# Kernel optimization log

Hardware: AMD Instinct MI355X
Metric: run time of the kernel (lower is better)

The kernel has to match this reference:

```python
import jax, jax.numpy as jnp
import numpy as np

# Geometry constants from System.__init__ defaults
L0, L1 = 0.4, 0.08                 # drone body half-extent basis lengths (l[0], l[1])
Y_LO, Y_HI = 0.0, 2.0              # y_limits
FAR = 10.0                         # sentinel 'no block ahead' distance
BLOCKS = np.array([[1.0, 0.9, 0.05, 0.4],
                   [2.5, 1.7, 0.05, 0.4],
                   [4.0, 0.4, 0.05, 0.4]], dtype=np.float32)  # [x, y, w, h]
B = 4_194_304                      # batch of environment states


def setup_inputs() -> dict:
    key = jax.random.key(0)
    u = jax.random.uniform(key, (B, 7), dtype=jnp.float32)
    # columns: c_x, c_y, v_x, v_y, phi, theta, wind -> scale to realistic ranges
    scale = jnp.array([5.0, 2.0, 4.0, 4.0, 1.0, 1.0, 2.4], dtype=jnp.float32)
    shift = jnp.array([0.0, 0.0, -2.0, -2.0, -0.5, -0.5, 5.5], dtype=jnp.float32)
    state = u * scale + shift
    blocks = jnp.asarray(BLOCKS)
    return {"state": state, "blocks": blocks}


def _get_observation(state, blocks):
    # state: [B, 7]; faithful vectorization of System.get_observation
    c_x, c_y, v_x, v_y, phi = (state[:, 0], state[:, 1], state[:, 2],
                               state[:, 3], state[:, 4])
    abs_phi = jnp.abs(phi)
    half_x = jnp.cos(phi) * L0 / 2 + jnp.sin(abs_phi) * L1 / 2   # horizontal half-extent
    half_y = jnp.sin(abs_phi) * L0 / 2 + jnp.cos(phi) * L1 / 2   # vertical half-extent

    up = Y_HI - c_y - half_y
    down = c_y - Y_LO - half_y
    d1 = jnp.full_like(c_x, FAR)
    d2 = jnp.full_like(c_x, FAR)

    # small fixed number of blocks -> unrolled loop; later blocks overwrite up/down
    # (matches torch loop order), while d1/d2 keep the FIRST passing block (d==10 guard).
    for i in range(blocks.shape[0]):
        x, y, w, h = blocks[i, 0], blocks[i, 1], blocks[i, 2], blocks[i, 3]
        lo, hi = c_x - half_x, c_x + half_x
        x_in = (((x - w / 2) <= hi) & ((x - w / 2) >= lo)) | \
               (((x + w / 2) <= hi) & ((x + w / 2) >= lo))
        up = jnp.where(x_in, y + h / 2 - c_y - half_y, up)
        down = jnp.where(x_in, c_y - (y - h / 2) - half_y, down)

        passed = hi < (x - w / 2)
        dist = x - w / 2 - c_x - half_x
        y1_out = ((c_y - half_y) < (y - h / 2)) | ((c_y - half_y) > (y + h / 2))
        y2_out = ((c_y + half_y) > (y + h / 2)) | ((c_y + half_y) < (y - h / 2))
        d1 = jnp.where(passed & y1_out & (d1 == FAR), dist, d1)
        d2 = jnp.where(passed & y2_out & (d2 == FAR), dist, d2)

    # torch: cat([d1,d2,up,down,v_x,v_y,phi], dim=0).t() -> [B, 7]
    return jnp.stack([d1, d2, up, down, v_x, v_y, phi], axis=1)


def reference(state, blocks):
    return _get_observation(state, blocks)
```

## Files before the change

### kernel.cpp

```cpp
#include <hip/hip_runtime.h>


namespace {
constexpr float kL0  = 0.4f;
constexpr float kL1  = 0.08f;
constexpr float kYLo = 0.0f;
constexpr float kYHi = 2.0f;
constexpr float kFar = 10.0f;
constexpr int COLS = 7;
constexpr int TPB  = 256;
constexpr int ROWS = 1024;
constexpr int RPT  = ROWS / TPB;
constexpr int TILE = ROWS * COLS;
}

template <bool EXACT>
__global__ __launch_bounds__(TPB) void obs_kernel(
    const float* __restrict__ state,
    const float* __restrict__ blocks,
    float* __restrict__ out,
    int nrows)
{
    __shared__ float lds[TILE];

    const int t = threadIdx.x;
    const long long ntot = (long long)nrows * COLS;
    const int ntiles = (nrows + ROWS - 1) / ROWS;

    float bxl[3], bxr[3], byb[3], byt[3];
    #pragma unroll
    for (int i = 0; i < 3; ++i) {
        const float x  = blocks[i * 4 + 0];
        const float y  = blocks[i * 4 + 1];
        const float w2 = 0.5f * blocks[i * 4 + 2];
        const float h2 = 0.5f * blocks[i * 4 + 3];
        bxl[i] = x - w2;
        bxr[i] = x + w2;
        byb[i] = y - h2;
        byt[i] = y + h2;
    }

    for (int tile = blockIdx.x; tile < ntiles; tile += gridDim.x) {
        const long long f0 = (long long)tile * TILE;

        #pragma unroll
        for (int k = 0; k < COLS; ++k) {
            const long long i4 = (f0 >> 2) + (long long)k * TPB + t;
            float4 v;
            if (EXACT) {
                v = reinterpret_cast<const float4*>(state)[i4];
            } else {
                const long long fe = i4 * 4;
                v = make_float4(0.f, 0.f, 0.f, 0.f);
                if (fe + 3 < ntot) {
                    v = reinterpret_cast<const float4*>(state)[i4];
                } else if (fe < ntot) {
                    float tmp[4] = {0.f, 0.f, 0.f, 0.f};
                    #pragma unroll
                    for (int j = 0; j < 4; ++j) if (fe + j < ntot) tmp[j] = state[fe + j];
                    v = make_float4(tmp[0], tmp[1], tmp[2], tmp[3]);
                }
            }
            reinterpret_cast<float4*>(lds)[k * TPB + t] = v;
        }
        __syncthreads();

        #pragma unroll
        for (int rr = 0; rr < RPT; ++rr) {
            float* s = &lds[(t + rr * TPB) * COLS];
            const float cx  = s[0];
            const float cy  = s[1];
            const float vx  = s[2];
            const float vy  = s[3];
            const float phi = s[4];

            float sa, ca;
            sincosf(fabsf(phi), &sa, &ca);
            const float half_x = ca * (kL0 * 0.5f) + sa * (kL1 * 0.5f);
            const float half_y = sa * (kL0 * 0.5f) + ca * (kL1 * 0.5f);

            float up   = kYHi - cy - half_y;
            float down = cy - kYLo - half_y;
            float d1 = kFar, d2 = kFar;
            const float lo = cx - half_x;
            const float hi = cx + half_x;
            const float ylo_e = cy - half_y;
            const float yhi_e = cy + half_y;

            #pragma unroll
            for (int i = 0; i < 3; ++i) {
                const bool x_in = (bxl[i] <= hi && bxl[i] >= lo) ||
                                  (bxr[i] <= hi && bxr[i] >= lo);
                if (x_in) {
                    up   = byt[i] - cy - half_y;
                    down = cy - byb[i] - half_y;
                }
                const bool passed = hi < bxl[i];
                const float dist  = bxl[i] - cx - half_x;
                const bool y1_out = (ylo_e < byb[i]) || (ylo_e > byt[i]);
                const bool y2_out = (yhi_e > byt[i]) || (yhi_e < byb[i]);
                if (passed && y1_out && d1 == kFar) d1 = dist;
                if (passed && y2_out && d2 == kFar) d2 = dist;
            }

            s[0] = d1;
            s[1] = d2;
            s[2] = up;
            s[3] = down;
            s[4] = vx;
            s[5] = vy;
            s[6] = phi;
        }
        __syncthreads();

        #pragma unroll
        for (int k = 0; k < COLS; ++k) {
            const long long i4 = (f0 >> 2) + (long long)k * TPB + t;
            const float4 v = reinterpret_cast<const float4*>(lds)[k * TPB + t];
            if (EXACT) {
                reinterpret_cast<float4*>(out)[i4] = v;
            } else {
                const long long fe = i4 * 4;
                if (fe + 3 < ntot) {
                    reinterpret_cast<float4*>(out)[i4] = v;
                } else if (fe < ntot) {
                    #pragma unroll
                    for (int j = 0; j < 4; ++j)
                        if (fe + j < ntot) out[fe + j] = (&v.x)[j];
                }
            }
        }
    }
}

extern "C" void kernel_launch(void* const* d_in, const int* in_sizes, int n_in,
                              void* d_out, int out_size, void* d_ws, size_t ws_size,
                              hipStream_t stream) {
    const float* state  = (const float*)d_in[0];
    const float* blocks = (const float*)d_in[1];
    float* out = (float*)d_out;

    const int nrows = in_sizes[0] / COLS;
    const int ntiles = (nrows + ROWS - 1) / ROWS;
    const int grid = ntiles < 4096 ? ntiles : 4096;

    if (nrows % ROWS == 0) {
        obs_kernel<true ><<<grid, TPB, 0, stream>>>(state, blocks, out, nrows);
    } else {
        obs_kernel<false><<<grid, TPB, 0, stream>>>(state, blocks, out, nrows);
    }
}
```

Before: 206.7 us.

## Replace LDS-staged coalesced tiles with direct per-row unaligned vector loads/stores

Removes the shared-memory staging of 1024-row tiles and the two block barriers. Each thread now reads its own 7-float row straight from global memory with an unaligned 4-wide load plus a scalar, and writes the result back with 4-wide, 2-wide and scalar stores, unrolled four rows per thread. This drops the LDS traffic and synchronization, but each thread now touches a row at a 28-byte stride, so wavefront accesses are less coalesced and may need more memory transactions.

```diff
diff --git a/kernel.cpp b/kernel.cpp
--- a/kernel.cpp
+++ b/kernel.cpp
@@ -9,23 +9,20 @@
 constexpr float kFar = 10.0f;
 constexpr int COLS = 7;
 constexpr int TPB  = 256;
-constexpr int ROWS = 1024;
-constexpr int RPT  = ROWS / TPB;
-constexpr int TILE = ROWS * COLS;
+constexpr int UNR  = 4;
 }
 
-template <bool EXACT>
+typedef float f4u __attribute__((ext_vector_type(4), aligned(4)));
+typedef float f2u __attribute__((ext_vector_type(2), aligned(4)));
+
 __global__ __launch_bounds__(TPB) void obs_kernel(
     const float* __restrict__ state,
     const float* __restrict__ blocks,
     float* __restrict__ out,
     int nrows)
 {
-    __shared__ float lds[TILE];
-
-    const int t = threadIdx.x;
-    const long long ntot = (long long)nrows * COLS;
-    const int ntiles = (nrows + ROWS - 1) / ROWS;
+    const int gtid = blockIdx.x * TPB + threadIdx.x;
+    const int NT   = gridDim.x * TPB;
 
     float bxl[3], bxr[3], byb[3], byt[3];
     #pragma unroll
@@ -40,39 +37,29 @@
         byt[i] = y + h2;
     }
 
-    for (int tile = blockIdx.x; tile < ntiles; tile += gridDim.x) {
-        const long long f0 = (long long)tile * TILE;
+    for (long long r0 = gtid; r0 < nrows; r0 += (long long)NT * UNR) {
+        f4u   a[UNR];
+        float ph[UNR];
+        #pragma unroll
+        for (int k = 0; k < UNR; ++k) {
+            const long long r = r0 + (long long)k * NT;
+            if (r < nrows) {
+                const float* p = state + r * COLS;
+                a[k]  = *reinterpret_cast<const f4u*>(p);
+                ph[k] = p[4];
+            }
+        }
 
         #pragma unroll
-        for (int k = 0; k < COLS; ++k) {
-            const long long i4 = (f0 >> 2) + (long long)k * TPB + t;
-            float4 v;
-            if (EXACT) {
-                v = reinterpret_cast<const float4*>(state)[i4];
-            } else {
-                const long long fe = i4 * 4;
-                v = make_float4(0.f, 0.f, 0.f, 0.f);
-                if (fe + 3 < ntot) {
-                    v = reinterpret_cast<const float4*>(state)[i4];
-                } else if (fe < ntot) {
-                    float tmp[4] = {0.f, 0.f, 0.f, 0.f};
-                    #pragma unroll
-                    for (int j = 0; j < 4; ++j) if (fe + j < ntot) tmp[j] = state[fe + j];
-                    v = make_float4(tmp[0], tmp[1], tmp[2], tmp[3]);
-                }
-            }
-            reinterpret_cast<float4*>(lds)[k * TPB + t] = v;
-        }
-        __syncthreads();
+        for (int k = 0; k < UNR; ++k) {
+            const long long r = r0 + (long long)k * NT;
+            if (r >= nrows) continue;
 
-        #pragma unroll
-        for (int rr = 0; rr < RPT; ++rr) {
-            float* s = &lds[(t + rr * TPB) * COLS];
-            const float cx  = s[0];
-            const float cy  = s[1];
-            const float vx  = s[2];
-            const float vy  = s[3];
-            const float phi = s[4];
+            const float cx  = a[k][0];
+            const float cy  = a[k][1];
+            const float vx  = a[k][2];
+            const float vy  = a[k][3];
+            const float phi = ph[k];
 
             float sa, ca;
             sincosf(fabsf(phi), &sa, &ca);
@@ -103,32 +90,12 @@
                 if (passed && y2_out && d2 == kFar) d2 = dist;
             }
 
-            s[0] = d1;
-            s[1] = d2;
-            s[2] = up;
-            s[3] = down;
-            s[4] = vx;
-            s[5] = vy;
-            s[6] = phi;
-        }
-        __syncthreads();
-
-        #pragma unroll
-        for (int k = 0; k < COLS; ++k) {
-            const long long i4 = (f0 >> 2) + (long long)k * TPB + t;
-            const float4 v = reinterpret_cast<const float4*>(lds)[k * TPB + t];
-            if (EXACT) {
-                reinterpret_cast<float4*>(out)[i4] = v;
-            } else {
-                const long long fe = i4 * 4;
-                if (fe + 3 < ntot) {
-                    reinterpret_cast<float4*>(out)[i4] = v;
-                } else if (fe < ntot) {
-                    #pragma unroll
-                    for (int j = 0; j < 4; ++j)
-                        if (fe + j < ntot) out[fe + j] = (&v.x)[j];
-                }
-            }
+            float* o = out + r * COLS;
+            f4u o4 = {d1, d2, up, down};
+            f2u o2 = {vx, vy};
+            *reinterpret_cast<f4u*>(o)     = o4;
+            *reinterpret_cast<f2u*>(o + 4) = o2;
+            o[6] = phi;
         }
     }
 }
@@ -141,12 +108,8 @@
     float* out = (float*)d_out;
 
     const int nrows = in_sizes[0] / COLS;
-    const int ntiles = (nrows + ROWS - 1) / ROWS;
-    const int grid = ntiles < 4096 ? ntiles : 4096;
+    long long want = ((long long)nrows + TPB * UNR - 1) / (TPB * UNR);
+    const int grid = (int)(want < 1 ? 1 : (want > 4096 ? 4096 : want));
 
-    if (nrows % ROWS == 0) {
-        obs_kernel<true ><<<grid, TPB, 0, stream>>>(state, blocks, out, nrows);
-    } else {
-        obs_kernel<false><<<grid, TPB, 0, stream>>>(state, blocks, out, nrows);
-    }
+    obs_kernel<<<grid, TPB, 0, stream>>>(state, blocks, out, nrows);
 }
```

After: 206.0 us. About the same (-0.3%).
